# Kernel optimization log

Hardware: AMD Instinct MI355X
Metric: run time of the kernel (lower is better)

The kernel has to match this reference:

```python
import jax, jax.numpy as jnp
import numpy as np

B, N, M = 1024, 65536, 128


def setup_inputs() -> dict:
    key = jax.random.key(0)
    k1, k2, k3, k4 = jax.random.split(key, 4)
    address = jax.random.uniform(k1, (B, N), dtype=jnp.float32)
    erase = jax.random.uniform(k2, (B, M), dtype=jnp.float32)
    add = jax.random.normal(k3, (B, M), dtype=jnp.float32)
    content = jax.random.uniform(k4, (N, M), dtype=jnp.float32)
    return {"address": address, "erase": erase, "add": add, "content": content}


def reference(address, erase, add, content):
    # write: outer-product erase/add aggregated over batch -> [N, M]
    erase_v = jnp.einsum('bn,bm->nm', address, erase)
    add_v = jnp.einsum('bn,bm->nm', address, add)
    new_content = content * (1.0 - erase_v) + add_v
    # read-after-write: [B,N] @ [N,M] -> [B,M]
    read_content = jnp.einsum('bn,nm->bm', address, new_content)
    return read_content
```

## Files before the change

### kernel.cpp

```cpp
#include <hip/hip_runtime.h>
#include <hip/hip_bf16.h>
#include <stdint.h>

#define B_SZ 1024
#define N_SZ 65536
#define M_SZ 128

typedef short bf16x8 __attribute__((ext_vector_type(8)));
typedef short bf16x4 __attribute__((ext_vector_type(4)));
typedef float f32x4 __attribute__((ext_vector_type(4)));

__device__ __forceinline__ unsigned short f2bf(float f) {
    uint32_t u = __float_as_uint(f);
    uint32_t r = (u + 0x7FFFu + ((u >> 16) & 1u)) >> 16;
    return (unsigned short)r;
}

__global__ __launch_bounds__(256) void k_edt(const float* __restrict__ E,
                                             const float* __restrict__ D,
                                             unsigned short* __restrict__ EDt) {
    __shared__ float tile[32][33];
    int bx = blockIdx.x & 31;
    int cy = blockIdx.x >> 5;
    int b0 = bx * 32, c0 = cy * 32;
    const float* src = (c0 < M_SZ) ? E : D;
    int cs0 = c0 & (M_SZ - 1);
    int t = threadIdx.x;
    int i = t >> 3, j = (t & 7) * 4;
    const float* p = src + (size_t)(b0 + i) * M_SZ + cs0 + j;
    float4 v = *(const float4*)p;
    tile[i][j] = v.x; tile[i][j + 1] = v.y; tile[i][j + 2] = v.z; tile[i][j + 3] = v.w;
    __syncthreads();
    int c = t >> 3, b4 = (t & 7) * 4;
    unsigned short* q = EDt + (size_t)(c0 + c) * B_SZ + b0 + b4;
    ushort4 o;
    o.x = f2bf(tile[b4 + 0][c]); o.y = f2bf(tile[b4 + 1][c]);
    o.z = f2bf(tile[b4 + 2][c]); o.w = f2bf(tile[b4 + 3][c]);
    *(ushort4*)q = o;
}

__global__ __launch_bounds__(256) void k_zero(float* __restrict__ out) {
    int i = blockIdx.x * 1024 + threadIdx.x * 4;
    *(float4*)(out + i) = (float4){0.f, 0.f, 0.f, 0.f};
}

#define AS_LD 132
#define ED_LD 40

__global__ __launch_bounds__(256, 2) void k_pass1(
    const float* __restrict__ A,
    const unsigned short* __restrict__ EDt,
    const float* __restrict__ C,
    unsigned short* __restrict__ NCt)
{
    __shared__ __align__(16) unsigned short As[2][32 * AS_LD];
    __shared__ __align__(16) unsigned short EDs[2][256 * ED_LD];
    const int t = threadIdx.x;
    const int lane = t & 63;
    const int wv = t >> 6;
    const int wvn = wv >> 1, wvc = wv & 1;
    const int g = lane >> 4;
    const int m16 = lane & 15;
    const int n0 = blockIdx.x * 128;

    const int kb = t >> 3;
    const int cA = (t & 7) * 16;
    const int colq = t >> 3;
    const int seg = t & 7;

    int cb[8];
#pragma unroll
    for (int fj = 0; fj < 4; ++fj) { cb[fj] = wvc * 4 + fj; cb[fj + 4] = 8 + wvc * 4 + fj; }

    f32x4 acc[4][8];
#pragma unroll
    for (int i = 0; i < 4; ++i)
#pragma unroll
        for (int j = 0; j < 8; ++j) acc[i][j] = (f32x4){0.f, 0.f, 0.f, 0.f};

    {
        const float* p = A + (size_t)kb * N_SZ + n0 + cA;
        float4 a0 = ((const float4*)p)[0], a1 = ((const float4*)p)[1];
        float4 a2 = ((const float4*)p)[2], a3 = ((const float4*)p)[3];
        ushort4* w = (ushort4*)&As[0][kb * AS_LD + cA];
        ushort4 o;
        o.x = f2bf(a0.x); o.y = f2bf(a0.y); o.z = f2bf(a0.z); o.w = f2bf(a0.w); w[0] = o;
        o.x = f2bf(a1.x); o.y = f2bf(a1.y); o.z = f2bf(a1.z); o.w = f2bf(a1.w); w[1] = o;
        o.x = f2bf(a2.x); o.y = f2bf(a2.y); o.z = f2bf(a2.z); o.w = f2bf(a2.w); w[2] = o;
        o.x = f2bf(a3.x); o.y = f2bf(a3.y); o.z = f2bf(a3.z); o.w = f2bf(a3.w); w[3] = o;
#pragma unroll
        for (int p8 = 0; p8 < 8; ++p8) {
            int col = p8 * 32 + colq;
            ushort4 v = *(const ushort4*)(EDt + (size_t)col * B_SZ + seg * 4);
            *(ushort4*)&EDs[0][col * ED_LD + seg * 4] = v;
        }
    }
    __syncthreads();

    int cur = 0;
    for (int bk = 0; bk < B_SZ; bk += 32) {
        const bool last = (bk + 32 >= B_SZ);
        const int nk = last ? 0 : bk + 32;

        const float* p = A + (size_t)(nk + kb) * N_SZ + n0 + cA;
        float4 a0 = ((const float4*)p)[0], a1 = ((const float4*)p)[1];
        float4 a2 = ((const float4*)p)[2], a3 = ((const float4*)p)[3];
        ushort4 e[8];
#pragma unroll
        for (int p8 = 0; p8 < 8; ++p8) {
            int col = p8 * 32 + colq;
            e[p8] = *(const ushort4*)(EDt + (size_t)col * B_SZ + nk + seg * 4);
        }

        bf16x8 af[4];
#pragma unroll
        for (int fi = 0; fi < 4; ++fi) {
            int nl = wvn * 64 + fi * 16 + m16;
#pragma unroll
            for (int j = 0; j < 8; ++j)
                af[fi][j] = (short)As[cur][(g * 8 + j) * AS_LD + nl];
        }
        bf16x8 bfr[8];
#pragma unroll
        for (int fj = 0; fj < 8; ++fj)
            bfr[fj] = *(const bf16x8*)&EDs[cur][(cb[fj] * 16 + m16) * ED_LD + g * 8];

#pragma unroll
        for (int fj = 0; fj < 8; ++fj)
#pragma unroll
            for (int fi = 0; fi < 4; ++fi)
                acc[fi][fj] = __builtin_amdgcn_mfma_f32_16x16x32_bf16(af[fi], bfr[fj], acc[fi][fj], 0, 0, 0);

        if (!last) {
            const int nxt = cur ^ 1;
            ushort4* w = (ushort4*)&As[nxt][kb * AS_LD + cA];
            ushort4 o;
            o.x = f2bf(a0.x); o.y = f2bf(a0.y); o.z = f2bf(a0.z); o.w = f2bf(a0.w); w[0] = o;
            o.x = f2bf(a1.x); o.y = f2bf(a1.y); o.z = f2bf(a1.z); o.w = f2bf(a1.w); w[1] = o;
            o.x = f2bf(a2.x); o.y = f2bf(a2.y); o.z = f2bf(a2.z); o.w = f2bf(a2.w); w[2] = o;
            o.x = f2bf(a3.x); o.y = f2bf(a3.y); o.z = f2bf(a3.z); o.w = f2bf(a3.w); w[3] = o;
#pragma unroll
            for (int p8 = 0; p8 < 8; ++p8) {
                int col = p8 * 32 + colq;
                *(ushort4*)&EDs[nxt][col * ED_LD + seg * 4] = e[p8];
            }
        }
        __syncthreads();
        cur ^= 1;
    }

#pragma unroll
    for (int fi = 0; fi < 4; ++fi)
#pragma unroll
        for (int fj = 0; fj < 4; ++fj) {
            int n_base = n0 + wvn * 64 + fi * 16 + g * 4;
            int m = wvc * 64 + fj * 16 + m16;
            bf16x4 o;
#pragma unroll
            for (int r = 0; r < 4; ++r) {
                float w = acc[fi][fj][r];
                float v = acc[fi][fj + 4][r];
                float cc = C[(size_t)(n_base + r) * M_SZ + m];
                o[r] = (short)f2bf(cc * (1.0f - w) + v);
            }
            *(bf16x4*)&NCt[(size_t)m * N_SZ + n_base] = o;
        }
}

#define L2_LD 40

__global__ __launch_bounds__(256, 2) void k_pass2(
    const float* __restrict__ A,
    const unsigned short* __restrict__ NCt,
    float* __restrict__ out)
{
    __shared__ __align__(16) unsigned short As2[2][128 * L2_LD];
    __shared__ __align__(16) unsigned short NCs[2][128 * L2_LD];
    const int t = threadIdx.x;
    const int lane = t & 63;
    const int wv = t >> 6;
    const int wvb = wv >> 1, wvm = wv & 1;
    const int g = lane >> 4;
    const int m16 = lane & 15;
    const int b0 = (blockIdx.x & 7) * 128;
    const int k0 = (blockIdx.x >> 3) * 1024;

    const int row = t >> 1, half = t & 1;

    f32x4 acc[4][4];
#pragma unroll
    for (int i = 0; i < 4; ++i)
#pragma unroll
        for (int j = 0; j < 4; ++j) acc[i][j] = (f32x4){0.f, 0.f, 0.f, 0.f};

    {
        const float* p = A + (size_t)(b0 + row) * N_SZ + k0 + half * 16;
        float4 a0 = ((const float4*)p)[0], a1 = ((const float4*)p)[1];
        float4 a2 = ((const float4*)p)[2], a3 = ((const float4*)p)[3];
        ushort4* w = (ushort4*)&As2[0][row * L2_LD + half * 16];
        ushort4 o;
        o.x = f2bf(a0.x); o.y = f2bf(a0.y); o.z = f2bf(a0.z); o.w = f2bf(a0.w); w[0] = o;
        o.x = f2bf(a1.x); o.y = f2bf(a1.y); o.z = f2bf(a1.z); o.w = f2bf(a1.w); w[1] = o;
        o.x = f2bf(a2.x); o.y = f2bf(a2.y); o.z = f2bf(a2.z); o.w = f2bf(a2.w); w[2] = o;
        o.x = f2bf(a3.x); o.y = f2bf(a3.y); o.z = f2bf(a3.z); o.w = f2bf(a3.w); w[3] = o;
        const uint4* pn = (const uint4*)(NCt + (size_t)row * N_SZ + k0 + half * 16);
        uint4 n0v = pn[0], n1v = pn[1];
        uint4* wn = (uint4*)&NCs[0][row * L2_LD + half * 16];
        wn[0] = n0v; wn[1] = n1v;
    }
    __syncthreads();

    int cur = 0;
    for (int kk = 0; kk < 1024; kk += 32) {
        const bool last = (kk + 32 >= 1024);
        const int nkk = last ? 0 : kk + 32;

        const float* p = A + (size_t)(b0 + row) * N_SZ + k0 + nkk + half * 16;
        float4 a0 = ((const float4*)p)[0], a1 = ((const float4*)p)[1];
        float4 a2 = ((const float4*)p)[2], a3 = ((const float4*)p)[3];
        const uint4* pn = (const uint4*)(NCt + (size_t)row * N_SZ + k0 + nkk + half * 16);
        uint4 n0v = pn[0], n1v = pn[1];

        bf16x8 af[4];
#pragma unroll
        for (int fi = 0; fi < 4; ++fi)
            af[fi] = *(const bf16x8*)&As2[cur][(wvb * 64 + fi * 16 + m16) * L2_LD + g * 8];
        bf16x8 bfr[4];
#pragma unroll
        for (int fj = 0; fj < 4; ++fj)
            bfr[fj] = *(const bf16x8*)&NCs[cur][(wvm * 64 + fj * 16 + m16) * L2_LD + g * 8];

#pragma unroll
        for (int fi = 0; fi < 4; ++fi)
#pragma unroll
            for (int fj = 0; fj < 4; ++fj)
                acc[fi][fj] = __builtin_amdgcn_mfma_f32_16x16x32_bf16(af[fi], bfr[fj], acc[fi][fj], 0, 0, 0);

        if (!last) {
            const int nxt = cur ^ 1;
            ushort4* w = (ushort4*)&As2[nxt][row * L2_LD + half * 16];
            ushort4 o;
            o.x = f2bf(a0.x); o.y = f2bf(a0.y); o.z = f2bf(a0.z); o.w = f2bf(a0.w); w[0] = o;
            o.x = f2bf(a1.x); o.y = f2bf(a1.y); o.z = f2bf(a1.z); o.w = f2bf(a1.w); w[1] = o;
            o.x = f2bf(a2.x); o.y = f2bf(a2.y); o.z = f2bf(a2.z); o.w = f2bf(a2.w); w[2] = o;
            o.x = f2bf(a3.x); o.y = f2bf(a3.y); o.z = f2bf(a3.z); o.w = f2bf(a3.w); w[3] = o;
            uint4* wn = (uint4*)&NCs[nxt][row * L2_LD + half * 16];
            wn[0] = n0v; wn[1] = n1v;
        }
        __syncthreads();
        cur ^= 1;
    }

#pragma unroll
    for (int fi = 0; fi < 4; ++fi)
#pragma unroll
        for (int fj = 0; fj < 4; ++fj)
#pragma unroll
            for (int r = 0; r < 4; ++r) {
                int b = b0 + wvb * 64 + fi * 16 + g * 4 + r;
                int m = wvm * 64 + fj * 16 + m16;
                atomicAdd(out + (size_t)b * M_SZ + m, acc[fi][fj][r]);
            }
}

extern "C" void kernel_launch(void* const* d_in, const int* in_sizes, int n_in,
                              void* d_out, int out_size, void* d_ws, size_t ws_size,
                              hipStream_t stream) {
    const float* A  = (const float*)d_in[0];
    const float* E  = (const float*)d_in[1];
    const float* Dd = (const float*)d_in[2];
    const float* C  = (const float*)d_in[3];
    float* out = (float*)d_out;

    unsigned short* NCt = (unsigned short*)d_ws;
    unsigned short* EDt = (unsigned short*)((char*)d_ws + (size_t)M_SZ * N_SZ * 2);

    k_edt <<<256, 256, 0, stream>>>(E, Dd, EDt);
    k_zero<<<128, 256, 0, stream>>>(out);
    k_pass1<<<512, 256, 0, stream>>>(A, EDt, C, NCt);
    k_pass2<<<512, 256, 0, stream>>>(A, NCt, out);
}
```

Baseline: 175.8 us.

## Swizzle pass1 A tile layout, deepen pass2 prefetch, fuse zero kernel, reorder blocks

Merges the output-zeroing kernel into the E/D transpose kernel as extra blocks, dropping one launch. In pass1 the A tile is stored as packed k-pairs in a swizzled 32-bit layout, so MFMA operands load as one 16-byte LDS read instead of eight scalar reads. In pass2 global loads are prefetched two chunks ahead in registers, and block indexing is reordered so consecutive blocks walk along N. The deeper prefetch raises register pressure, and the swizzle adds index arithmetic on the stores.

```diff
diff --git a/kernel.cpp b/kernel.cpp
--- a/kernel.cpp
+++ b/kernel.cpp
@@ -18,7 +18,13 @@
 
 __global__ __launch_bounds__(256) void k_edt(const float* __restrict__ E,
                                              const float* __restrict__ D,
-                                             unsigned short* __restrict__ EDt) {
+                                             unsigned short* __restrict__ EDt,
+                                             float* __restrict__ out) {
+    if (blockIdx.x >= 256) {
+        int i = (blockIdx.x - 256) * 1024 + threadIdx.x * 4;
+        *(float4*)(out + i) = (float4){0.f, 0.f, 0.f, 0.f};
+        return;
+    }
     __shared__ float tile[32][33];
     int bx = blockIdx.x & 31;
     int cy = blockIdx.x >> 5;
@@ -39,13 +45,13 @@
     *(ushort4*)q = o;
 }
 
-__global__ __launch_bounds__(256) void k_zero(float* __restrict__ out) {
-    int i = blockIdx.x * 1024 + threadIdx.x * 4;
-    *(float4*)(out + i) = (float4){0.f, 0.f, 0.f, 0.f};
-}
-
-#define AS_LD 132
+#define AS_U32 (128 * 20)
 #define ED_LD 40
+
+__device__ __forceinline__ int a_swz(int n, int p) {
+    int s = ((n >> 2) ^ (n >> 4)) & 3;
+    return n * 20 + (p ^ (s << 2));
+}
 
 __global__ __launch_bounds__(256, 2) void k_pass1(
     const float* __restrict__ A,
@@ -53,7 +59,7 @@
     const float* __restrict__ C,
     unsigned short* __restrict__ NCt)
 {
-    __shared__ __align__(16) unsigned short As[2][32 * AS_LD];
+    __shared__ __align__(16) uint32_t As32[2][AS_U32];
     __shared__ __align__(16) unsigned short EDs[2][256 * ED_LD];
     const int t = threadIdx.x;
     const int lane = t & 63;
@@ -63,8 +69,8 @@
     const int m16 = lane & 15;
     const int n0 = blockIdx.x * 128;
 
-    const int kb = t >> 3;
-    const int cA = (t & 7) * 16;
+    const int pp = t >> 4;
+    const int sub = t & 15;
     const int colq = t >> 3;
     const int seg = t & 7;
 
@@ -79,15 +85,18 @@
         for (int j = 0; j < 8; ++j) acc[i][j] = (f32x4){0.f, 0.f, 0.f, 0.f};
 
     {
-        const float* p = A + (size_t)kb * N_SZ + n0 + cA;
-        float4 a0 = ((const float4*)p)[0], a1 = ((const float4*)p)[1];
-        float4 a2 = ((const float4*)p)[2], a3 = ((const float4*)p)[3];
-        ushort4* w = (ushort4*)&As[0][kb * AS_LD + cA];
-        ushort4 o;
-        o.x = f2bf(a0.x); o.y = f2bf(a0.y); o.z = f2bf(a0.z); o.w = f2bf(a0.w); w[0] = o;
-        o.x = f2bf(a1.x); o.y = f2bf(a1.y); o.z = f2bf(a1.z); o.w = f2bf(a1.w); w[1] = o;
-        o.x = f2bf(a2.x); o.y = f2bf(a2.y); o.z = f2bf(a2.z); o.w = f2bf(a2.w); w[2] = o;
-        o.x = f2bf(a3.x); o.y = f2bf(a3.y); o.z = f2bf(a3.z); o.w = f2bf(a3.w); w[3] = o;
+        const float* r0 = A + (size_t)(2 * pp) * N_SZ + n0 + sub * 8;
+        const float* r1 = r0 + N_SZ;
+        float4 a0 = ((const float4*)r0)[0], a1 = ((const float4*)r0)[1];
+        float4 b0v = ((const float4*)r1)[0], b1v = ((const float4*)r1)[1];
+        float r0v[8] = {a0.x,a0.y,a0.z,a0.w,a1.x,a1.y,a1.z,a1.w};
+        float r1v[8] = {b0v.x,b0v.y,b0v.z,b0v.w,b1v.x,b1v.y,b1v.z,b1v.w};
+#pragma unroll
+        for (int j = 0; j < 8; ++j) {
+            int n = sub * 8 + j;
+            uint32_t v = (uint32_t)f2bf(r0v[j]) | ((uint32_t)f2bf(r1v[j]) << 16);
+            As32[0][a_swz(n, pp)] = v;
+        }
 #pragma unroll
         for (int p8 = 0; p8 < 8; ++p8) {
             int col = p8 * 32 + colq;
@@ -102,9 +111,10 @@
         const bool last = (bk + 32 >= B_SZ);
         const int nk = last ? 0 : bk + 32;
 
-        const float* p = A + (size_t)(nk + kb) * N_SZ + n0 + cA;
-        float4 a0 = ((const float4*)p)[0], a1 = ((const float4*)p)[1];
-        float4 a2 = ((const float4*)p)[2], a3 = ((const float4*)p)[3];
+        const float* r0 = A + (size_t)(nk + 2 * pp) * N_SZ + n0 + sub * 8;
+        const float* r1 = r0 + N_SZ;
+        float4 a0 = ((const float4*)r0)[0], a1 = ((const float4*)r0)[1];
+        float4 b0v = ((const float4*)r1)[0], b1v = ((const float4*)r1)[1];
         ushort4 e[8];
 #pragma unroll
         for (int p8 = 0; p8 < 8; ++p8) {
@@ -115,10 +125,9 @@
         bf16x8 af[4];
 #pragma unroll
         for (int fi = 0; fi < 4; ++fi) {
-            int nl = wvn * 64 + fi * 16 + m16;
-#pragma unroll
-            for (int j = 0; j < 8; ++j)
-                af[fi][j] = (short)As[cur][(g * 8 + j) * AS_LD + nl];
+            int n = wvn * 64 + fi * 16 + m16;
+            int s = ((n >> 2) ^ (n >> 4)) & 3;
+            af[fi] = *(const bf16x8*)&As32[cur][n * 20 + ((g ^ s) << 2)];
         }
         bf16x8 bfr[8];
 #pragma unroll
@@ -133,12 +142,14 @@
 
         if (!last) {
             const int nxt = cur ^ 1;
-            ushort4* w = (ushort4*)&As[nxt][kb * AS_LD + cA];
-            ushort4 o;
-            o.x = f2bf(a0.x); o.y = f2bf(a0.y); o.z = f2bf(a0.z); o.w = f2bf(a0.w); w[0] = o;
-            o.x = f2bf(a1.x); o.y = f2bf(a1.y); o.z = f2bf(a1.z); o.w = f2bf(a1.w); w[1] = o;
-            o.x = f2bf(a2.x); o.y = f2bf(a2.y); o.z = f2bf(a2.z); o.w = f2bf(a2.w); w[2] = o;
-            o.x = f2bf(a3.x); o.y = f2bf(a3.y); o.z = f2bf(a3.z); o.w = f2bf(a3.w); w[3] = o;
+            float r0v[8] = {a0.x,a0.y,a0.z,a0.w,a1.x,a1.y,a1.z,a1.w};
+            float r1v[8] = {b0v.x,b0v.y,b0v.z,b0v.w,b1v.x,b1v.y,b1v.z,b1v.w};
+#pragma unroll
+            for (int j = 0; j < 8; ++j) {
+                int n = sub * 8 + j;
+                uint32_t v = (uint32_t)f2bf(r0v[j]) | ((uint32_t)f2bf(r1v[j]) << 16);
+                As32[nxt][a_swz(n, pp)] = v;
+            }
 #pragma unroll
             for (int p8 = 0; p8 < 8; ++p8) {
                 int col = p8 * 32 + colq;
@@ -168,6 +179,7 @@
 }
 
 #define L2_LD 40
+#define NCHUNK 32
 
 __global__ __launch_bounds__(256, 2) void k_pass2(
     const float* __restrict__ A,
@@ -182,8 +194,8 @@
     const int wvb = wv >> 1, wvm = wv & 1;
     const int g = lane >> 4;
     const int m16 = lane & 15;
-    const int b0 = (blockIdx.x & 7) * 128;
-    const int k0 = (blockIdx.x >> 3) * 1024;
+    const int k0 = (blockIdx.x & 63) << 10;
+    const int b0 = (7 - (blockIdx.x >> 6)) << 7;
 
     const int row = t >> 1, half = t & 1;
 
@@ -193,62 +205,65 @@
 #pragma unroll
         for (int j = 0; j < 4; ++j) acc[i][j] = (f32x4){0.f, 0.f, 0.f, 0.f};
 
+    float4 ra[2][4];
+    uint4  rn[2][2];
+
+#pragma unroll
+    for (int c = 0; c < 2; ++c) {
+        const float* p = A + (size_t)(b0 + row) * N_SZ + k0 + c * 32 + half * 16;
+        ra[c][0] = ((const float4*)p)[0]; ra[c][1] = ((const float4*)p)[1];
+        ra[c][2] = ((const float4*)p)[2]; ra[c][3] = ((const float4*)p)[3];
+        const uint4* pn = (const uint4*)(NCt + (size_t)row * N_SZ + k0 + c * 32 + half * 16);
+        rn[c][0] = pn[0]; rn[c][1] = pn[1];
+    }
     {
-        const float* p = A + (size_t)(b0 + row) * N_SZ + k0 + half * 16;
-        float4 a0 = ((const float4*)p)[0], a1 = ((const float4*)p)[1];
-        float4 a2 = ((const float4*)p)[2], a3 = ((const float4*)p)[3];
         ushort4* w = (ushort4*)&As2[0][row * L2_LD + half * 16];
         ushort4 o;
-        o.x = f2bf(a0.x); o.y = f2bf(a0.y); o.z = f2bf(a0.z); o.w = f2bf(a0.w); w[0] = o;
-        o.x = f2bf(a1.x); o.y = f2bf(a1.y); o.z = f2bf(a1.z); o.w = f2bf(a1.w); w[1] = o;
-        o.x = f2bf(a2.x); o.y = f2bf(a2.y); o.z = f2bf(a2.z); o.w = f2bf(a2.w); w[2] = o;
-        o.x = f2bf(a3.x); o.y = f2bf(a3.y); o.z = f2bf(a3.z); o.w = f2bf(a3.w); w[3] = o;
-        const uint4* pn = (const uint4*)(NCt + (size_t)row * N_SZ + k0 + half * 16);
-        uint4 n0v = pn[0], n1v = pn[1];
+        o.x = f2bf(ra[0][0].x); o.y = f2bf(ra[0][0].y); o.z = f2bf(ra[0][0].z); o.w = f2bf(ra[0][0].w); w[0] = o;
+        o.x = f2bf(ra[0][1].x); o.y = f2bf(ra[0][1].y); o.z = f2bf(ra[0][1].z); o.w = f2bf(ra[0][1].w); w[1] = o;
+        o.x = f2bf(ra[0][2].x); o.y = f2bf(ra[0][2].y); o.z = f2bf(ra[0][2].z); o.w = f2bf(ra[0][2].w); w[2] = o;
+        o.x = f2bf(ra[0][3].x); o.y = f2bf(ra[0][3].y); o.z = f2bf(ra[0][3].z); o.w = f2bf(ra[0][3].w); w[3] = o;
         uint4* wn = (uint4*)&NCs[0][row * L2_LD + half * 16];
-        wn[0] = n0v; wn[1] = n1v;
+        wn[0] = rn[0][0]; wn[1] = rn[0][1];
     }
     __syncthreads();
 
-    int cur = 0;
-    for (int kk = 0; kk < 1024; kk += 32) {
-        const bool last = (kk + 32 >= 1024);
-        const int nkk = last ? 0 : kk + 32;
-
-        const float* p = A + (size_t)(b0 + row) * N_SZ + k0 + nkk + half * 16;
-        float4 a0 = ((const float4*)p)[0], a1 = ((const float4*)p)[1];
-        float4 a2 = ((const float4*)p)[2], a3 = ((const float4*)p)[3];
-        const uint4* pn = (const uint4*)(NCt + (size_t)row * N_SZ + k0 + nkk + half * 16);
-        uint4 n0v = pn[0], n1v = pn[1];
+#pragma unroll 2
+    for (int c = 0; c < NCHUNK; ++c) {
+        if (c + 2 < NCHUNK) {
+            const float* p = A + (size_t)(b0 + row) * N_SZ + k0 + (c + 2) * 32 + half * 16;
+            ra[c & 1][0] = ((const float4*)p)[0]; ra[c & 1][1] = ((const float4*)p)[1];
+            ra[c & 1][2] = ((const float4*)p)[2]; ra[c & 1][3] = ((const float4*)p)[3];
+            const uint4* pn = (const uint4*)(NCt + (size_t)row * N_SZ + k0 + (c + 2) * 32 + half * 16);
+            rn[c & 1][0] = pn[0]; rn[c & 1][1] = pn[1];
+        }
 
         bf16x8 af[4];
 #pragma unroll
         for (int fi = 0; fi < 4; ++fi)
-            af[fi] = *(const bf16x8*)&As2[cur][(wvb * 64 + fi * 16 + m16) * L2_LD + g * 8];
+            af[fi] = *(const bf16x8*)&As2[c & 1][(wvb * 64 + fi * 16 + m16) * L2_LD + g * 8];
         bf16x8 bfr[4];
 #pragma unroll
         for (int fj = 0; fj < 4; ++fj)
-            bfr[fj] = *(const bf16x8*)&NCs[cur][(wvm * 64 + fj * 16 + m16) * L2_LD + g * 8];
-
+            bfr[fj] = *(const bf16x8*)&NCs[c & 1][(wvm * 64 + fj * 16 + m16) * L2_LD + g * 8];
 #pragma unroll
         for (int fi = 0; fi < 4; ++fi)
 #pragma unroll
             for (int fj = 0; fj < 4; ++fj)
                 acc[fi][fj] = __builtin_amdgcn_mfma_f32_16x16x32_bf16(af[fi], bfr[fj], acc[fi][fj], 0, 0, 0);
 
-        if (!last) {
-            const int nxt = cur ^ 1;
-            ushort4* w = (ushort4*)&As2[nxt][row * L2_LD + half * 16];
+        if (c + 1 < NCHUNK) {
+            const int s = (c + 1) & 1;
+            ushort4* w = (ushort4*)&As2[s][row * L2_LD + half * 16];
             ushort4 o;
-            o.x = f2bf(a0.x); o.y = f2bf(a0.y); o.z = f2bf(a0.z); o.w = f2bf(a0.w); w[0] = o;
-            o.x = f2bf(a1.x); o.y = f2bf(a1.y); o.z = f2bf(a1.z); o.w = f2bf(a1.w); w[1] = o;
-            o.x = f2bf(a2.x); o.y = f2bf(a2.y); o.z = f2bf(a2.z); o.w = f2bf(a2.w); w[2] = o;
-            o.x = f2bf(a3.x); o.y = f2bf(a3.y); o.z = f2bf(a3.z); o.w = f2bf(a3.w); w[3] = o;
-            uint4* wn = (uint4*)&NCs[nxt][row * L2_LD + half * 16];
-            wn[0] = n0v; wn[1] = n1v;
+            o.x = f2bf(ra[s][0].x); o.y = f2bf(ra[s][0].y); o.z = f2bf(ra[s][0].z); o.w = f2bf(ra[s][0].w); w[0] = o;
+            o.x = f2bf(ra[s][1].x); o.y = f2bf(ra[s][1].y); o.z = f2bf(ra[s][1].z); o.w = f2bf(ra[s][1].w); w[1] = o;
+            o.x = f2bf(ra[s][2].x); o.y = f2bf(ra[s][2].y); o.z = f2bf(ra[s][2].z); o.w = f2bf(ra[s][2].w); w[2] = o;
+            o.x = f2bf(ra[s][3].x); o.y = f2bf(ra[s][3].y); o.z = f2bf(ra[s][3].z); o.w = f2bf(ra[s][3].w); w[3] = o;
+            uint4* wn = (uint4*)&NCs[s][row * L2_LD + half * 16];
+            wn[0] = rn[s][0]; wn[1] = rn[s][1];
         }
         __syncthreads();
-        cur ^= 1;
     }
 
 #pragma unroll
@@ -275,8 +290,7 @@
     unsigned short* NCt = (unsigned short*)d_ws;
     unsigned short* EDt = (unsigned short*)((char*)d_ws + (size_t)M_SZ * N_SZ * 2);
 
-    k_edt <<<256, 256, 0, stream>>>(E, Dd, EDt);
-    k_zero<<<128, 256, 0, stream>>>(out);
+    k_edt <<<384, 256, 0, stream>>>(E, Dd, EDt, out);
     k_pass1<<<512, 256, 0, stream>>>(A, EDt, C, NCt);
     k_pass2<<<512, 256, 0, stream>>>(A, NCt, out);
 }
```

Measured after the change: 186.4 us. 6.1% more time.
